# Optimization experiments

Hardware: AMD Instinct MI355X
Metric: run time of the kernel (lower is better)

The kernel has to match this reference:

```python
import jax, jax.numpy as jnp
import numpy as np

N_SAMPLES = 200            # points sampled per ray (n_points in source)
T_HASH = 1 << 19           # hash table size per level (log2_hashmap_size=19)
_PRIMES = jnp.array([1, 2654435761, 805459861], dtype=jnp.uint32)
_CORNERS = jnp.array([[i, j, k] for i in (0, 1) for j in (0, 1) for k in (0, 1)], dtype=jnp.int32)  # [8,3]


def sample_points_along_ray(start, end):
    # start/end: [B,2] in [0,1]. Lerp xy along the ray, z = normalized depth t.
    t = jnp.linspace(0.0, 1.0, N_SAMPLES, dtype=start.dtype)           # [S]
    xy = start[:, None, :] * (1.0 - t)[None, :, None] + end[:, None, :] * t[None, :, None]  # [B,S,2]
    z = jnp.broadcast_to(t[None, :, None], (start.shape[0], N_SAMPLES, 1))
    return jnp.concatenate([xy, z], axis=-1)                            # [B,S,3]


def grid_encode(pts, tables, base_res):
    # pts: [N,3] in [0,1]; tables: [L, T_HASH, D]. Multi-res hash grid + trilinear interp.
    L = tables.shape[0]
    outs = []
    for l in range(L):
        res = base_res * (2 ** l)
        xf = pts * res
        x0 = jnp.floor(xf).astype(jnp.int32)
        w = xf - x0                                                     # [N,3] trilinear weights
        c = x0[:, None, :] + _CORNERS[None]                             # [N,8,3]
        h = c.astype(jnp.uint32) * _PRIMES[None, None, :]
        idx = (h[..., 0] ^ h[..., 1] ^ h[..., 2]) & jnp.uint32(T_HASH - 1)  # [N,8]
        cw = jnp.prod(jnp.where(_CORNERS[None].astype(bool), w[:, None, :], 1.0 - w[:, None, :]), axis=-1)  # [N,8]
        feat = tables[l][idx.astype(jnp.int32)]                         # [N,8,D] gather
        outs.append(jnp.sum(feat * cw[..., None], axis=1))              # [N,D]
    return jnp.concatenate(outs, axis=-1)


def setup_inputs() -> dict:
    key = jax.random.key(0)
    ks = jax.random.split(key, 13)
    B = 16384
    return {
        "x": jax.random.uniform(ks[0], (B, 4), dtype=jnp.float32),
        "table_label": jax.random.normal(ks[1], (5, T_HASH, 1), dtype=jnp.float32),
        "table_rgb": jax.random.normal(ks[2], (6, T_HASH, 4), dtype=jnp.float32),
        "w_label": jax.random.normal(ks[3], (5, 1), dtype=jnp.float32),
        "b_label": jax.random.normal(ks[4], (1,), dtype=jnp.float32),
        "W1": jax.random.normal(ks[5], (120, 64), dtype=jnp.float32) * 0.1,
        "b1": jax.random.normal(ks[6], (64,), dtype=jnp.float32) * 0.1,
        "W2": jax.random.normal(ks[7], (64, 64), dtype=jnp.float32) * 0.1,
        "b2": jax.random.normal(ks[8], (64,), dtype=jnp.float32) * 0.1,
        "W3": jax.random.normal(ks[9], (64, 64), dtype=jnp.float32) * 0.1,
        "b3": jax.random.normal(ks[10], (64,), dtype=jnp.float32) * 0.1,
        "W4": jax.random.normal(ks[11], (64, 3), dtype=jnp.float32) * 0.1,
        "b4": jax.random.normal(ks[12], (3,), dtype=jnp.float32) * 0.1,
    }


def reference(x, table_label, table_rgb, w_label, b_label, W1, b1, W2, b2, W3, b3, W4, b4):
    B = x.shape[0]
    pts = sample_points_along_ray(x[:, :2], x[:, 2:4]).reshape(-1, 3)   # [B*S,3]
    enc_l = grid_encode(pts, table_label, 8).reshape(B, N_SAMPLES, -1)  # [B,S,5]
    label = jax.nn.sigmoid(enc_l @ w_label + b_label)                   # [B,S,1]
    hits = jnp.max(label, axis=1)                                       # [B,1]
    first = jnp.argmax((label > 0.5).astype(jnp.float32), axis=1).reshape(-1)  # [B]
    enc_r = grid_encode(pts, table_rgb, 4).reshape(B, N_SAMPLES, -1)    # [B,S,24]
    rows = jnp.arange(B)
    maxi = N_SAMPLES - 1

    def gather(off):
        return enc_r[rows, jnp.clip(first + off, 0, maxi)]              # [B,24]

    feat = jnp.concatenate([gather(-2), gather(-1), gather(0), gather(1), gather(2)], axis=-1)  # [B,120]
    h = jax.nn.relu(feat @ W1 + b1)
    h = jax.nn.relu(h @ W2 + b2)
    h = jax.nn.relu(h @ W3 + b3)
    rgb = h @ W4 + b4                                                   # [B,3]
    return hits, label, rgb
```

## Files before the change

kernel.cpp:

```cpp
#include <hip/hip_runtime.h>
#include <math.h>
#include <stdint.h>

#define NS 200
#define THASH (1 << 19)
#define TMASK ((1u << 19) - 1u)

__device__ __forceinline__ float sigmoidf_(float v) {
    return 1.0f / (1.0f + __expf(-v));
}

__global__ __launch_bounds__(256) void k_label(
        const float* __restrict__ x,
        const float* __restrict__ tlab,
        const float* __restrict__ wlab, const float* __restrict__ blab,
        float* __restrict__ hits, float* __restrict__ labels,
        int* __restrict__ firsts)
{
    const uint32_t P2 = 2654435761u, P3 = 805459861u;
    const int b = blockIdx.x;
    const int tid = threadIdx.x;
    const int lane = tid & 63;
    const int wid = tid >> 6;
    const float4 ray = *(const float4*)(x + 4 * (size_t)b);

    const int s_eff = tid < NS ? tid : NS - 1;
    const float t = (float)s_eff * (1.0f / 199.0f);
    const float px = ray.x * (1.0f - t) + ray.z * t;
    const float py = ray.y * (1.0f - t) + ray.w * t;
    const float pz = t;

    const float xf4 = px * 128.0f, yf4 = py * 128.0f, zf4 = pz * 128.0f;
    const float fx4 = floorf(xf4), fy4 = floorf(yf4), fz4 = floorf(zf4);
    const uint32_t x4 = (uint32_t)(int)fx4;
    const uint32_t y4 = (uint32_t)(int)fy4;
    const uint32_t z4 = (uint32_t)(int)fz4;
    const uint32_t cell4 = x4 | (y4 << 10) | (z4 << 20);
    const uint32_t prev = __shfl_up(cell4, 1);
    const uint32_t diff = cell4 ^ prev;

    float acc = blab[0];

    #pragma unroll
    for (int l = 0; l < 4; ++l) {
        const int k = 4 - l;
        const uint32_t fm = 0x3FFu & ~((1u << k) - 1u);
        const uint32_t m_l = fm | (fm << 10) | (fm << 20);
        const bool leader = (lane == 0) || ((diff & m_l) != 0u);
        const uint64_t bal = __ballot(leader);
        const uint64_t below = bal & (~0ull >> (63 - lane));
        const int ldr = 63 - __clzll(below);

        const uint32_t x0 = x4 >> k, y0 = y4 >> k, z0 = z4 >> k;
        const float sc = 1.0f / (float)(1 << k);
        const float wx = fmaf(xf4, sc, -(float)x0);
        const float wy = fmaf(yf4, sc, -(float)y0);
        const float wz = fmaf(zf4, sc, -(float)z0);

        float v0 = 0.f, v1 = 0.f, v2 = 0.f, v3 = 0.f,
              v4v = 0.f, v5 = 0.f, v6 = 0.f, v7 = 0.f;
        if (leader) {
            const uint32_t hy0 = y0 * P2, hz0 = z0 * P3;
            const uint32_t base = x0 ^ hy0 ^ hz0;
            const uint32_t dx = x0 ^ (x0 + 1u);
            const uint32_t dy = hy0 ^ (hy0 + P2);
            const uint32_t dz = hz0 ^ (hz0 + P3);
            const float* __restrict__ tl = tlab + (size_t)l * THASH;
            v0  = tl[ base                 & TMASK];
            v1  = tl[(base ^ dz)           & TMASK];
            v2  = tl[(base ^ dy)           & TMASK];
            v3  = tl[(base ^ dy ^ dz)      & TMASK];
            v4v = tl[(base ^ dx)           & TMASK];
            v5  = tl[(base ^ dx ^ dz)      & TMASK];
            v6  = tl[(base ^ dx ^ dy)      & TMASK];
            v7  = tl[(base ^ dx ^ dy ^ dz) & TMASK];
        }
        v0  = __shfl(v0, ldr);  v1 = __shfl(v1, ldr);
        v2  = __shfl(v2, ldr);  v3 = __shfl(v3, ldr);
        v4v = __shfl(v4v, ldr); v5 = __shfl(v5, ldr);
        v6  = __shfl(v6, ldr);  v7 = __shfl(v7, ldr);

        const float c00 = fmaf(wz, v1 - v0, v0);
        const float c01 = fmaf(wz, v3 - v2, v2);
        const float c10 = fmaf(wz, v5 - v4v, v4v);
        const float c11 = fmaf(wz, v7 - v6, v6);
        const float c0 = fmaf(wy, c01 - c00, c00);
        const float c1 = fmaf(wy, c11 - c10, c10);
        const float cv = fmaf(wx, c1 - c0, c0);
        acc = fmaf(cv, wlab[l], acc);
    }

    {
        const float wx = xf4 - fx4, wy = yf4 - fy4, wz = zf4 - fz4;
        const uint32_t hy0 = y4 * P2, hz0 = z4 * P3;
        const uint32_t base = x4 ^ hy0 ^ hz0;
        const uint32_t dx = x4 ^ (x4 + 1u);
        const uint32_t dy = hy0 ^ (hy0 + P2);
        const uint32_t dz = hz0 ^ (hz0 + P3);
        const float* __restrict__ tl = tlab + (size_t)4 * THASH;
        const float v0  = tl[ base                 & TMASK];
        const float v1  = tl[(base ^ dz)           & TMASK];
        const float v2  = tl[(base ^ dy)           & TMASK];
        const float v3  = tl[(base ^ dy ^ dz)      & TMASK];
        const float v4v = tl[(base ^ dx)           & TMASK];
        const float v5  = tl[(base ^ dx ^ dz)      & TMASK];
        const float v6  = tl[(base ^ dx ^ dy)      & TMASK];
        const float v7  = tl[(base ^ dx ^ dy ^ dz) & TMASK];
        const float c00 = fmaf(wz, v1 - v0, v0);
        const float c01 = fmaf(wz, v3 - v2, v2);
        const float c10 = fmaf(wz, v5 - v4v, v4v);
        const float c11 = fmaf(wz, v7 - v6, v6);
        const float c0 = fmaf(wy, c01 - c00, c00);
        const float c1 = fmaf(wy, c11 - c10, c10);
        const float cv = fmaf(wx, c1 - c0, c0);
        acc = fmaf(cv, wlab[4], acc);
    }

    float lab = -1.0f;
    int cand = NS;
    if (tid < NS) {
        lab = sigmoidf_(acc);
        labels[(size_t)b * NS + tid] = lab;
        if (lab > 0.5f) cand = tid;
    }

    __shared__ float wmax[4];
    __shared__ int wmin[4];
    float m = lab;
    int c = cand;
    #pragma unroll
    for (int off = 32; off > 0; off >>= 1) {
        m = fmaxf(m, __shfl_xor(m, off));
        c = min(c, __shfl_xor(c, off));
    }
    if (lane == 0) { wmax[wid] = m; wmin[wid] = c; }
    __syncthreads();
    if (tid == 0) {
        float mm = fmaxf(fmaxf(wmax[0], wmax[1]), fmaxf(wmax[2], wmax[3]));
        int cc = min(min(wmin[0], wmin[1]), min(wmin[2], wmin[3]));
        hits[b] = mm;
        firsts[b] = (cc >= NS) ? 0 : cc;
    }
}

#define RPB 16
__global__ __launch_bounds__(256) void k_rgb(
        const float* __restrict__ x,
        const float* __restrict__ trgb,
        const int* __restrict__ firsts,
        const float* __restrict__ W1, const float* __restrict__ b1,
        const float* __restrict__ W2, const float* __restrict__ b2,
        const float* __restrict__ W3, const float* __restrict__ b3,
        const float* __restrict__ W4, const float* __restrict__ b4,
        float* __restrict__ rgb)
{
    const uint32_t P2 = 2654435761u, P3 = 805459861u;
    const int tid = threadIdx.x;
    const int lane = tid & 63;
    const int wid = tid >> 6;
    const int rayBase = blockIdx.x * RPB;

    __shared__ float feat[RPB][120];
    __shared__ float hs[RPB][64];

    const int corner = tid & 7;
    const int rp = tid >> 3;
    const int ray = rp >> 1;
    const int pairHalf = rp & 1;
    const int bi = (corner >> 2) & 1, bj = (corner >> 1) & 1, bk = corner & 1;

    const float4 rd = *(const float4*)(x + 4 * (size_t)(rayBase + ray));
    const int first = firsts[rayBase + ray];

    #pragma unroll
    for (int it = 0; it < 15; ++it) {
        const int pair = pairHalf * 15 + it;
        const int si = pair / 6;
        const int l = pair % 6;
        int scl = first + si - 2;
        scl = scl < 0 ? 0 : (scl > NS - 1 ? NS - 1 : scl);
        const float t = (float)scl * (1.0f / 199.0f);
        const float px = rd.x * (1.0f - t) + rd.z * t;
        const float py = rd.y * (1.0f - t) + rd.w * t;
        const float pz = t;
        const int res = 4 << l;
        const float xf = px * (float)res, yf = py * (float)res, zf = pz * (float)res;
        const float fx = floorf(xf), fy = floorf(yf), fz = floorf(zf);
        const float wx = xf - fx, wy = yf - fy, wz = zf - fz;
        const uint32_t x0 = (uint32_t)(int)fx, y0 = (uint32_t)(int)fy, z0 = (uint32_t)(int)fz;
        const uint32_t hx = x0 + (uint32_t)bi;
        const uint32_t hy = (y0 + (uint32_t)bj) * P2;
        const uint32_t hz = (z0 + (uint32_t)bk) * P3;
        const uint32_t idx = (hx ^ hy ^ hz) & TMASK;
        const float cw = (bi ? wx : 1.0f - wx) * (bj ? wy : 1.0f - wy) * (bk ? wz : 1.0f - wz);
        const float4 tv = *(const float4*)(trgb + (((size_t)l << 19) + idx) * 4);
        float vx = tv.x * cw, vy = tv.y * cw, vz = tv.z * cw, vw = tv.w * cw;
        #pragma unroll
        for (int mm = 1; mm < 8; mm <<= 1) {
            vx += __shfl_xor(vx, mm);
            vy += __shfl_xor(vy, mm);
            vz += __shfl_xor(vz, mm);
            vw += __shfl_xor(vw, mm);
        }
        if (corner == 0) {
            float* f = &feat[ray][si * 24 + l * 4];
            f[0] = vx; f[1] = vy; f[2] = vz; f[3] = vw;
        }
    }
    __syncthreads();

    const int r0 = wid * 4;

    float a0 = b1[lane], a1 = a0, a2 = a0, a3 = a0;
    #pragma unroll 6
    for (int i = 0; i < 120; i += 4) {
        const float4 f0 = *(const float4*)(&feat[r0 + 0][i]);
        const float4 f1 = *(const float4*)(&feat[r0 + 1][i]);
        const float4 f2 = *(const float4*)(&feat[r0 + 2][i]);
        const float4 f3 = *(const float4*)(&feat[r0 + 3][i]);
        #pragma unroll
        for (int j = 0; j < 4; ++j) {
            const float wv = W1[(i + j) * 64 + lane];
            a0 = fmaf(((const float*)&f0)[j], wv, a0);
            a1 = fmaf(((const float*)&f1)[j], wv, a1);
            a2 = fmaf(((const float*)&f2)[j], wv, a2);
            a3 = fmaf(((const float*)&f3)[j], wv, a3);
        }
    }
    hs[r0 + 0][lane] = fmaxf(a0, 0.f);
    hs[r0 + 1][lane] = fmaxf(a1, 0.f);
    hs[r0 + 2][lane] = fmaxf(a2, 0.f);
    hs[r0 + 3][lane] = fmaxf(a3, 0.f);
    __syncthreads();

    a0 = b2[lane]; a1 = a0; a2 = a0; a3 = a0;
    #pragma unroll 4
    for (int i = 0; i < 64; i += 4) {
        const float4 f0 = *(const float4*)(&hs[r0 + 0][i]);
        const float4 f1 = *(const float4*)(&hs[r0 + 1][i]);
        const float4 f2 = *(const float4*)(&hs[r0 + 2][i]);
        const float4 f3 = *(const float4*)(&hs[r0 + 3][i]);
        #pragma unroll
        for (int j = 0; j < 4; ++j) {
            const float wv = W2[(i + j) * 64 + lane];
            a0 = fmaf(((const float*)&f0)[j], wv, a0);
            a1 = fmaf(((const float*)&f1)[j], wv, a1);
            a2 = fmaf(((const float*)&f2)[j], wv, a2);
            a3 = fmaf(((const float*)&f3)[j], wv, a3);
        }
    }
    __syncthreads();
    hs[r0 + 0][lane] = fmaxf(a0, 0.f);
    hs[r0 + 1][lane] = fmaxf(a1, 0.f);
    hs[r0 + 2][lane] = fmaxf(a2, 0.f);
    hs[r0 + 3][lane] = fmaxf(a3, 0.f);
    __syncthreads();

    a0 = b3[lane]; a1 = a0; a2 = a0; a3 = a0;
    #pragma unroll 4
    for (int i = 0; i < 64; i += 4) {
        const float4 f0 = *(const float4*)(&hs[r0 + 0][i]);
        const float4 f1 = *(const float4*)(&hs[r0 + 1][i]);
        const float4 f2 = *(const float4*)(&hs[r0 + 2][i]);
        const float4 f3 = *(const float4*)(&hs[r0 + 3][i]);
        #pragma unroll
        for (int j = 0; j < 4; ++j) {
            const float wv = W3[(i + j) * 64 + lane];
            a0 = fmaf(((const float*)&f0)[j], wv, a0);
            a1 = fmaf(((const float*)&f1)[j], wv, a1);
            a2 = fmaf(((const float*)&f2)[j], wv, a2);
            a3 = fmaf(((const float*)&f3)[j], wv, a3);
        }
    }
    __syncthreads();
    hs[r0 + 0][lane] = fmaxf(a0, 0.f);
    hs[r0 + 1][lane] = fmaxf(a1, 0.f);
    hs[r0 + 2][lane] = fmaxf(a2, 0.f);
    hs[r0 + 3][lane] = fmaxf(a3, 0.f);
    __syncthreads();

    if (lane < 12) {
        const int r = lane / 3, ch = lane % 3;
        float acc = b4[ch];
        #pragma unroll 8
        for (int j = 0; j < 64; ++j)
            acc = fmaf(hs[r0 + r][j], W4[j * 3 + ch], acc);
        rgb[(size_t)(rayBase + r0 + r) * 3 + ch] = acc;
    }
}

extern "C" void kernel_launch(void* const* d_in, const int* in_sizes, int n_in,
                              void* d_out, int out_size, void* d_ws, size_t ws_size,
                              hipStream_t stream) {
    const float* x    = (const float*)d_in[0];
    const float* tlab = (const float*)d_in[1];
    const float* trgb = (const float*)d_in[2];
    const float* wlab = (const float*)d_in[3];
    const float* blab = (const float*)d_in[4];
    const float* W1   = (const float*)d_in[5];
    const float* b1   = (const float*)d_in[6];
    const float* W2   = (const float*)d_in[7];
    const float* b2   = (const float*)d_in[8];
    const float* W3   = (const float*)d_in[9];
    const float* b3   = (const float*)d_in[10];
    const float* W4   = (const float*)d_in[11];
    const float* b4   = (const float*)d_in[12];

    const int B = in_sizes[0] / 4;

    float* hits   = (float*)d_out;
    float* labels = hits + B;
    float* rgbout = labels + (size_t)B * NS;
    int* firsts   = (int*)d_ws;

    k_label<<<B, 256, 0, stream>>>(x, tlab, wlab, blab, hits, labels, firsts);
    k_rgb<<<B / RPB, 256, 0, stream>>>(x, trgb, firsts,
                                       W1, b1, W2, b2, W3, b3, W4, b4, rgbout);
}
```

Measured before the change: 106.2 us.

## Compact coarse-level hash gathers into per-wave LDS queue, widen rgb blocks

For the three coarsest label levels, the leader lanes of each wave write their cell hash descriptors into a shared-memory queue. The whole wave then performs the 8-corner gathers together, one corner per lane, and stores the values to LDS, where every lane reads its cell's corners. This replaces the divergent per-leader 8-load sequence, which left most lanes idle, with dense gather issue, at the cost of about 30KB of LDS per block and some extra address arithmetic. Separately, the rgb kernel processes 32 rays per 512-thread block instead of 16 per 256, which relies on the unseen kernel body scaling with RPB and the new block size.

```diff
diff --git a/kernel.cpp b/kernel.cpp
--- a/kernel.cpp
+++ b/kernel.cpp
@@ -5,6 +5,7 @@
 #define NS 200
 #define THASH (1 << 19)
 #define TMASK ((1u << 19) - 1u)
+#define QCAP 192
 
 __device__ __forceinline__ float sigmoidf_(float v) {
     return 1.0f / (1.0f + __expf(-v));
@@ -22,8 +23,13 @@
     const int tid = threadIdx.x;
     const int lane = tid & 63;
     const int wid = tid >> 6;
+
+    __shared__ uint4 q[4][QCAP];
+    __shared__ float vbuf[4][QCAP * 8];
+    __shared__ float wmax[4];
+    __shared__ int wmin[4];
+
     const float4 ray = *(const float4*)(x + 4 * (size_t)b);
-
     const int s_eff = tid < NS ? tid : NS - 1;
     const float t = (float)s_eff * (1.0f / 199.0f);
     const float px = ray.x * (1.0f - t) + ray.z * t;
@@ -39,33 +45,107 @@
     const uint32_t prev = __shfl_up(cell4, 1);
     const uint32_t diff = cell4 ^ prev;
 
+    const uint64_t mask_excl = (1ull << lane) - 1ull;
+    const uint64_t mask_incl = mask_excl | (1ull << lane);
+
+    bool led[3];
+    int ldr[3], gslot[3];
+    int S;
+    {
+        uint64_t bal0, bal1, bal2;
+        #define LFLAG(L, K, BAL) { \
+            const uint32_t fm = 0x3FFu & ~((1u << (K)) - 1u); \
+            const uint32_t m_l = fm | (fm << 10) | (fm << 20); \
+            led[L] = (lane == 0) || ((diff & m_l) != 0u); \
+            BAL = __ballot(led[L]); \
+            ldr[L] = 63 - __clzll(BAL & mask_incl); }
+        LFLAG(0, 4, bal0)
+        LFLAG(1, 3, bal1)
+        LFLAG(2, 2, bal2)
+        #undef LFLAG
+        const int S0 = __popcll(bal0);
+        const int S1 = __popcll(bal1);
+        gslot[0] = __popcll(bal0 & mask_excl);
+        gslot[1] = S0 + __popcll(bal1 & mask_excl);
+        gslot[2] = S0 + S1 + __popcll(bal2 & mask_excl);
+        S = S0 + S1 + __popcll(bal2);
+    }
+
+    #pragma unroll
+    for (int l = 0; l < 3; ++l) {
+        if (led[l]) {
+            const int k = 4 - l;
+            const uint32_t x0 = x4 >> k, y0 = y4 >> k, z0 = z4 >> k;
+            const uint32_t hy0 = y0 * P2, hz0 = z0 * P3;
+            const uint32_t base = x0 ^ hy0 ^ hz0;
+            const uint32_t dxl = (x0 ^ (x0 + 1u)) | ((uint32_t)l << 24);
+            const uint32_t dy = hy0 ^ (hy0 + P2);
+            const uint32_t dz = hz0 ^ (hz0 + P3);
+            q[wid][gslot[l]] = make_uint4(base, dxl, dy, dz);
+        }
+    }
+
+    {
+        const int corner = lane & 7;
+        const int sub = lane >> 3;
+        const int nIt = (S + 7) >> 3;
+        for (int it = 0; it < nIt; ++it) {
+            const int e = it * 8 + sub;
+            const bool valid = e < S;
+            const uint4 ent = q[wid][valid ? e : 0];
+            uint32_t idx = ent.x;
+            if (corner & 4) idx ^= (ent.y & 0x00FFFFFFu);
+            if (corner & 2) idx ^= ent.z;
+            if (corner & 1) idx ^= ent.w;
+            const uint32_t lvl = ent.y >> 24;
+            const float v = tlab[((size_t)lvl << 19) + (idx & TMASK)];
+            if (valid) vbuf[wid][e * 8 + corner] = v;
+        }
+    }
+
     float acc = blab[0];
-
     #pragma unroll
-    for (int l = 0; l < 4; ++l) {
+    for (int l = 0; l < 3; ++l) {
         const int k = 4 - l;
-        const uint32_t fm = 0x3FFu & ~((1u << k) - 1u);
-        const uint32_t m_l = fm | (fm << 10) | (fm << 20);
-        const bool leader = (lane == 0) || ((diff & m_l) != 0u);
-        const uint64_t bal = __ballot(leader);
-        const uint64_t below = bal & (~0ull >> (63 - lane));
-        const int ldr = 63 - __clzll(below);
-
         const uint32_t x0 = x4 >> k, y0 = y4 >> k, z0 = z4 >> k;
         const float sc = 1.0f / (float)(1 << k);
         const float wx = fmaf(xf4, sc, -(float)x0);
         const float wy = fmaf(yf4, sc, -(float)y0);
         const float wz = fmaf(zf4, sc, -(float)z0);
+        const int ms = __shfl(gslot[l], ldr[l]);
+        const float4 lo = *(const float4*)&vbuf[wid][ms * 8];
+        const float4 hi = *(const float4*)&vbuf[wid][ms * 8 + 4];
+        const float c00 = fmaf(wz, lo.y - lo.x, lo.x);
+        const float c01 = fmaf(wz, lo.w - lo.z, lo.z);
+        const float c10 = fmaf(wz, hi.y - hi.x, hi.x);
+        const float c11 = fmaf(wz, hi.w - hi.z, hi.z);
+        const float c0 = fmaf(wy, c01 - c00, c00);
+        const float c1 = fmaf(wy, c11 - c10, c10);
+        const float cv = fmaf(wx, c1 - c0, c0);
+        acc = fmaf(cv, wlab[l], acc);
+    }
+
+    {
+        const uint32_t fm = 0x3FFu & ~1u;
+        const uint32_t m_l = fm | (fm << 10) | (fm << 20);
+        const bool led3 = (lane == 0) || ((diff & m_l) != 0u);
+        const uint64_t bal3 = __ballot(led3);
+        const int ldr3 = 63 - __clzll(bal3 & mask_incl);
+
+        const uint32_t x0 = x4 >> 1, y0 = y4 >> 1, z0 = z4 >> 1;
+        const float wx = fmaf(xf4, 0.5f, -(float)x0);
+        const float wy = fmaf(yf4, 0.5f, -(float)y0);
+        const float wz = fmaf(zf4, 0.5f, -(float)z0);
 
         float v0 = 0.f, v1 = 0.f, v2 = 0.f, v3 = 0.f,
               v4v = 0.f, v5 = 0.f, v6 = 0.f, v7 = 0.f;
-        if (leader) {
+        if (led3) {
             const uint32_t hy0 = y0 * P2, hz0 = z0 * P3;
             const uint32_t base = x0 ^ hy0 ^ hz0;
             const uint32_t dx = x0 ^ (x0 + 1u);
             const uint32_t dy = hy0 ^ (hy0 + P2);
             const uint32_t dz = hz0 ^ (hz0 + P3);
-            const float* __restrict__ tl = tlab + (size_t)l * THASH;
+            const float* __restrict__ tl = tlab + (size_t)3 * THASH;
             v0  = tl[ base                 & TMASK];
             v1  = tl[(base ^ dz)           & TMASK];
             v2  = tl[(base ^ dy)           & TMASK];
@@ -75,10 +155,10 @@
             v6  = tl[(base ^ dx ^ dy)      & TMASK];
             v7  = tl[(base ^ dx ^ dy ^ dz) & TMASK];
         }
-        v0  = __shfl(v0, ldr);  v1 = __shfl(v1, ldr);
-        v2  = __shfl(v2, ldr);  v3 = __shfl(v3, ldr);
-        v4v = __shfl(v4v, ldr); v5 = __shfl(v5, ldr);
-        v6  = __shfl(v6, ldr);  v7 = __shfl(v7, ldr);
+        v0  = __shfl(v0, ldr3);  v1 = __shfl(v1, ldr3);
+        v2  = __shfl(v2, ldr3);  v3 = __shfl(v3, ldr3);
+        v4v = __shfl(v4v, ldr3); v5 = __shfl(v5, ldr3);
+        v6  = __shfl(v6, ldr3);  v7 = __shfl(v7, ldr3);
 
         const float c00 = fmaf(wz, v1 - v0, v0);
         const float c01 = fmaf(wz, v3 - v2, v2);
@@ -87,7 +167,7 @@
         const float c0 = fmaf(wy, c01 - c00, c00);
         const float c1 = fmaf(wy, c11 - c10, c10);
         const float cv = fmaf(wx, c1 - c0, c0);
-        acc = fmaf(cv, wlab[l], acc);
+        acc = fmaf(cv, wlab[3], acc);
     }
 
     {
@@ -124,8 +204,6 @@
         if (lab > 0.5f) cand = tid;
     }
 
-    __shared__ float wmax[4];
-    __shared__ int wmin[4];
     float m = lab;
     int c = cand;
     #pragma unroll
@@ -143,8 +221,8 @@
     }
 }
 
-#define RPB 16
-__global__ __launch_bounds__(256) void k_rgb(
+#define RPB 32
+__global__ __launch_bounds__(512) void k_rgb(
         const float* __restrict__ x,
         const float* __restrict__ trgb,
         const int* __restrict__ firsts,
@@ -314,6 +392,6 @@
     int* firsts   = (int*)d_ws;
 
     k_label<<<B, 256, 0, stream>>>(x, tlab, wlab, blab, hits, labels, firsts);
-    k_rgb<<<B / RPB, 256, 0, stream>>>(x, trgb, firsts,
+    k_rgb<<<B / RPB, 512, 0, stream>>>(x, trgb, firsts,
                                        W1, b1, W2, b2, W3, b3, W4, b4, rgbout);
 }
```

New measurement: 108.8 us. 1.02x slower.
